# Kernel tuning notes

Measured on AMD Instinct MI355X. Metric: run time of the kernel, lower is better.

## Reference

```python
import jax, jax.numpy as jnp
import numpy as np

NUM_CLASSES = 1000
SCALE = 1.0

def setup_inputs() -> dict:
    key = jax.random.key(0)
    x = jax.random.normal(key, (32768, NUM_CLASSES), dtype=jnp.float32)
    return {"input": x}

def reference(input) -> jnp.ndarray:
    # residual defaults to input in the torch module
    r = input                                   # [B, C]
    n = NUM_CLASSES
    ra = jnp.abs(r)
    mean = jnp.mean(ra, axis=-1, keepdims=True)
    std = jnp.std(ra, axis=-1, keepdims=True, ddof=1)  # torch.std is unbiased
    w = SCALE * jax.nn.sigmoid((ra - mean) / std)       # [B, C]
    # W = I + 1/(n-1) * diag(w) @ (ones - n*I);  (W r)_i = r_i + w_i/(n-1)*(sum(r) - n*r_i)
    s = jnp.sum(r, axis=-1, keepdims=True)              # [B, 1]
    out = r + w / (n - 1) * (s - n * r)
    return out
```

## Files before the change

kernel.cpp:

```cpp
#include <hip/hip_runtime.h>
#include <math.h>

#define NC 1000
#define NV 250

__device__ __forceinline__ float sigmoidf(float x) {
    return 1.0f / (1.0f + expf(-x));
}

__global__ __launch_bounds__(256)
void smooth_filter_kernel(const float* __restrict__ in, float* __restrict__ out) {
    const int row  = blockIdx.x;
    const int t    = threadIdx.x;
    const int wave = t >> 6;
    const int lane = t & 63;

    const float4* __restrict__ rp = (const float4*)(in + (size_t)row * NC);

    float4 v = make_float4(0.f, 0.f, 0.f, 0.f);
    if (t < NV) v = rp[t];

    const float a0 = fabsf(v.x), a1 = fabsf(v.y), a2 = fabsf(v.z), a3 = fabsf(v.w);

    float s_r  = (v.x + v.y) + (v.z + v.w);
    float s_a  = (a0 + a1) + (a2 + a3);
    float s_a2 = (a0 * a0 + a1 * a1) + (a2 * a2 + a3 * a3);

    #pragma unroll
    for (int off = 32; off > 0; off >>= 1) {
        s_r  += __shfl_down(s_r,  off, 64);
        s_a  += __shfl_down(s_a,  off, 64);
        s_a2 += __shfl_down(s_a2, off, 64);
    }

    __shared__ float red[3][4];
    if (lane == 0) {
        red[0][wave] = s_r;
        red[1][wave] = s_a;
        red[2][wave] = s_a2;
    }
    __syncthreads();

    const float S   = (red[0][0] + red[0][1]) + (red[0][2] + red[0][3]);
    const float SA  = (red[1][0] + red[1][1]) + (red[1][2] + red[1][3]);
    const float SA2 = (red[2][0] + red[2][1]) + (red[2][2] + red[2][3]);

    const float mean    = SA * (1.0f / NC);
    const float var     = (SA2 - (float)NC * mean * mean) * (1.0f / (NC - 1));
    const float inv_std = rsqrtf(var);
    const float c       = 1.0f / (NC - 1);

    if (t < NV) {
        float4 o;
        o.x = v.x + sigmoidf((a0 - mean) * inv_std) * c * (S - (float)NC * v.x);
        o.y = v.y + sigmoidf((a1 - mean) * inv_std) * c * (S - (float)NC * v.y);
        o.z = v.z + sigmoidf((a2 - mean) * inv_std) * c * (S - (float)NC * v.z);
        o.w = v.w + sigmoidf((a3 - mean) * inv_std) * c * (S - (float)NC * v.w);
        ((float4*)(out + (size_t)row * NC))[t] = o;
    }
}

extern "C" void kernel_launch(void* const* d_in, const int* in_sizes, int n_in,
                              void* d_out, int out_size, void* d_ws, size_t ws_size,
                              hipStream_t stream) {
    const float* in  = (const float*)d_in[0];
    float*       out = (float*)d_out;
    const int rows   = in_sizes[0] / NC;
    smooth_filter_kernel<<<rows, 256, 0, stream>>>(in, out);
}
```

Baseline: 216.3 us.

## Map one row per wavefront with shuffle-only reduction and nontemporal stores

Each 64-lane wavefront now owns a full row and loads four float4 vectors per lane, with four rows per block. The row reduction becomes a pure xor-shuffle butterfly, which removes the shared-memory staging and __syncthreads. The sigmoid switches to __expf, and outputs use nontemporal stores to avoid polluting cache. In exchange, each lane holds more registers, and the fast exp slightly lowers accuracy.

```diff
diff --git a/kernel.cpp b/kernel.cpp
--- a/kernel.cpp
+++ b/kernel.cpp
@@ -1,62 +1,63 @@
 #include <hip/hip_runtime.h>
 #include <math.h>
 
-#define NC 1000
-#define NV 250
+#define NC   1000
+#define NV4  250
+#define RPB  4
 
-__device__ __forceinline__ float sigmoidf(float x) {
-    return 1.0f / (1.0f + expf(-x));
+typedef float fvec4 __attribute__((ext_vector_type(4)));
+
+__device__ __forceinline__ float fast_sigmoid(float x) {
+    return 1.0f / (1.0f + __expf(-x));
 }
 
 __global__ __launch_bounds__(256)
-void smooth_filter_kernel(const float* __restrict__ in, float* __restrict__ out) {
-    const int row  = blockIdx.x;
-    const int t    = threadIdx.x;
-    const int wave = t >> 6;
-    const int lane = t & 63;
+void smooth_filter_kernel(const float* __restrict__ in, float* __restrict__ out, int nrows) {
+    const int wave = threadIdx.x >> 6;
+    const int lane = threadIdx.x & 63;
+    const int row  = blockIdx.x * RPB + wave;
+    if (row >= nrows) return;
 
-    const float4* __restrict__ rp = (const float4*)(in + (size_t)row * NC);
+    const fvec4* __restrict__ rp = (const fvec4*)(in  + (size_t)row * NC);
+    fvec4*       __restrict__ wp = (fvec4*)      (out + (size_t)row * NC);
 
-    float4 v = make_float4(0.f, 0.f, 0.f, 0.f);
-    if (t < NV) v = rp[t];
-
-    const float a0 = fabsf(v.x), a1 = fabsf(v.y), a2 = fabsf(v.z), a3 = fabsf(v.w);
-
-    float s_r  = (v.x + v.y) + (v.z + v.w);
-    float s_a  = (a0 + a1) + (a2 + a3);
-    float s_a2 = (a0 * a0 + a1 * a1) + (a2 * a2 + a3 * a3);
+    fvec4 v[4];
+    float s_r = 0.f, s_a = 0.f, s_a2 = 0.f;
+    #pragma unroll
+    for (int j = 0; j < 4; ++j) {
+        const int idx = lane + 64 * j;
+        v[j] = (fvec4)(0.f);
+        if (idx < NV4) v[j] = rp[idx];
+        const float a0 = fabsf(v[j].x), a1 = fabsf(v[j].y),
+                    a2 = fabsf(v[j].z), a3 = fabsf(v[j].w);
+        s_r  += (v[j].x + v[j].y) + (v[j].z + v[j].w);
+        s_a  += (a0 + a1) + (a2 + a3);
+        s_a2 += (a0 * a0 + a1 * a1) + (a2 * a2 + a3 * a3);
+    }
 
     #pragma unroll
-    for (int off = 32; off > 0; off >>= 1) {
-        s_r  += __shfl_down(s_r,  off, 64);
-        s_a  += __shfl_down(s_a,  off, 64);
-        s_a2 += __shfl_down(s_a2, off, 64);
+    for (int m = 32; m > 0; m >>= 1) {
+        s_r  += __shfl_xor(s_r,  m, 64);
+        s_a  += __shfl_xor(s_a,  m, 64);
+        s_a2 += __shfl_xor(s_a2, m, 64);
     }
 
-    __shared__ float red[3][4];
-    if (lane == 0) {
-        red[0][wave] = s_r;
-        red[1][wave] = s_a;
-        red[2][wave] = s_a2;
-    }
-    __syncthreads();
-
-    const float S   = (red[0][0] + red[0][1]) + (red[0][2] + red[0][3]);
-    const float SA  = (red[1][0] + red[1][1]) + (red[1][2] + red[1][3]);
-    const float SA2 = (red[2][0] + red[2][1]) + (red[2][2] + red[2][3]);
-
-    const float mean    = SA * (1.0f / NC);
-    const float var     = (SA2 - (float)NC * mean * mean) * (1.0f / (NC - 1));
+    const float mean    = s_a * (1.0f / NC);
+    const float var     = (s_a2 - (float)NC * mean * mean) * (1.0f / (NC - 1));
     const float inv_std = rsqrtf(var);
     const float c       = 1.0f / (NC - 1);
 
-    if (t < NV) {
-        float4 o;
-        o.x = v.x + sigmoidf((a0 - mean) * inv_std) * c * (S - (float)NC * v.x);
-        o.y = v.y + sigmoidf((a1 - mean) * inv_std) * c * (S - (float)NC * v.y);
-        o.z = v.z + sigmoidf((a2 - mean) * inv_std) * c * (S - (float)NC * v.z);
-        o.w = v.w + sigmoidf((a3 - mean) * inv_std) * c * (S - (float)NC * v.w);
-        ((float4*)(out + (size_t)row * NC))[t] = o;
+    #pragma unroll
+    for (int j = 0; j < 4; ++j) {
+        const int idx = lane + 64 * j;
+        if (idx < NV4) {
+            fvec4 o;
+            o.x = v[j].x + fast_sigmoid((fabsf(v[j].x) - mean) * inv_std) * c * (s_r - (float)NC * v[j].x);
+            o.y = v[j].y + fast_sigmoid((fabsf(v[j].y) - mean) * inv_std) * c * (s_r - (float)NC * v[j].y);
+            o.z = v[j].z + fast_sigmoid((fabsf(v[j].z) - mean) * inv_std) * c * (s_r - (float)NC * v[j].z);
+            o.w = v[j].w + fast_sigmoid((fabsf(v[j].w) - mean) * inv_std) * c * (s_r - (float)NC * v[j].w);
+            __builtin_nontemporal_store(o, wp + idx);
+        }
     }
 }
 
@@ -65,6 +66,7 @@
                               hipStream_t stream) {
     const float* in  = (const float*)d_in[0];
     float*       out = (float*)d_out;
-    const int rows   = in_sizes[0] / NC;
-    smooth_filter_kernel<<<rows, 256, 0, stream>>>(in, out);
+    const int nrows  = in_sizes[0] / NC;
+    const int blocks = (nrows + RPB - 1) / RPB;
+    smooth_filter_kernel<<<blocks, 256, 0, stream>>>(in, out, nrows);
 }
```

Result: slower. 226.5 us (+4.7%).
